# Kernel optimization log

Measured on AMD Instinct MI355X. Metric: run time of the kernel, lower is better.

## Reference

```python
import jax, jax.numpy as jnp
import numpy as np

HW = 128  # BEV heatmap size hardcoded in the module

def conv2d(x, w, b, pad):
    y = jax.lax.conv_general_dilated(x, w, (1, 1), [(pad, pad), (pad, pad)],
                                     dimension_numbers=('NCHW', 'OIHW', 'NCHW'))
    return y + b[None, :, None, None]

def setup_inputs() -> dict:
    key = jax.random.key(0)
    ks = jax.random.split(key, 8)
    B, C, N = 4, 64, 4096
    middle_feat_lidar = jax.random.normal(ks[0], (B, C, HW, HW), dtype=jnp.float32)
    voxels_feat_radar = jax.random.normal(ks[1], (N, C), dtype=jnp.float32)
    rcoors = jax.random.randint(ks[2], (N, 4), 0, HW, dtype=jnp.int64)
    rcoors = rcoors.at[:, 0].set(rcoors[:, 0] % B)  # batch index in [0, B)
    rcs = jax.random.uniform(ks[3], (N,), dtype=jnp.float32) * 6.0
    gamma = jnp.array(1.0, dtype=jnp.float32)  # self.rcs_gamma
    # rcs_att: Conv2d(2, C, 1); compress: Conv2d(2C, C, 3, pad=1)
    att_w = jax.random.normal(ks[4], (C, 2, 1, 1), dtype=jnp.float32) * 0.5
    att_b = jnp.zeros((C,), dtype=jnp.float32)
    comp_w = jax.random.normal(ks[5], (C, 2 * C, 3, 3), dtype=jnp.float32) * (1.0 / np.sqrt(2 * C * 9))
    comp_b = jnp.zeros((C,), dtype=jnp.float32)
    return {"middle_feat_lidar": middle_feat_lidar, "voxels_feat_radar": voxels_feat_radar,
            "rcoors": rcoors, "batch_size": B, "rcs": rcs, "gamma": gamma,
            "att_w": att_w, "att_b": att_b, "comp_w": comp_w, "comp_b": comp_b}

def _draw_maps(rcoors, rcs, gamma, batch_size):
    # Vectorized CenterPoint-style gaussian scatter-max over all N points.
    true_rcs = jax.nn.relu(rcs)                      # (N,)
    r = jnp.floor(gamma * true_rcs + 1.0)            # int() truncation; radius >= 1
    sigma = (2.0 * r + 1.0) / 6.0                    # sigma = diameter / 6
    b = rcoors[:, 0]
    y = rcoors[:, 2].astype(jnp.float32)
    x = rcoors[:, 3].astype(jnp.float32)
    grid = jnp.arange(HW, dtype=jnp.float32)
    dy = grid[None, :] - y[:, None]                  # (N, HW) rows
    dx = grid[None, :] - x[:, None]                  # (N, HW) cols
    g = jnp.exp(-(dy[:, :, None] ** 2 + dx[:, None, :] ** 2)
                / (2.0 * sigma[:, None, None] ** 2))  # (N, HW, HW)
    eps = jnp.finfo(jnp.float32).eps
    g = jnp.where(g < eps, 0.0, g)                   # gaussian_2d eps cutoff (max is 1 at center)
    # truncate gaussian to its (2r+1) box, as the slicing in draw_heatmap_gaussian does
    box = (jnp.abs(dy[:, :, None]) <= r[:, None, None]) & (jnp.abs(dx[:, None, :]) <= r[:, None, None])
    g = jnp.where(box, g, 0.0)
    heatmap = jnp.maximum(jax.ops.segment_max(g, b, num_segments=batch_size), 0.0)          # (B,HW,HW)
    heatmap_feat = jnp.maximum(
        jax.ops.segment_max(g * true_rcs[:, None, None], b, num_segments=batch_size), 0.0)  # (B,HW,HW)
    return heatmap, heatmap_feat

def reference(middle_feat_lidar, voxels_feat_radar, rcoors, batch_size, rcs,
              gamma, att_w, att_b, comp_w, comp_b):
    heatmap, heatmap_feat = _draw_maps(rcoors, rcs, gamma, batch_size)
    hm2 = jnp.stack([heatmap, heatmap_feat], axis=1)        # (B,2,HW,HW)
    rcs_features = conv2d(hm2, att_w, att_b, pad=0)          # 1x1 conv
    fused = jnp.concatenate([middle_feat_lidar, rcs_features], axis=1)
    return conv2d(fused, comp_w, comp_b, pad=1)              # 3x3 conv
```

## Files before the change

### kernel.cpp

```cpp
#include <hip/hip_runtime.h>
#include <math.h>

#define HW 128
#define CCH 64

typedef unsigned short u16;
typedef __attribute__((ext_vector_type(8))) short bf16x8;
typedef __attribute__((ext_vector_type(4))) float f32x4;

static __device__ __forceinline__ u16 f2bf(float x) {
    unsigned int u = __float_as_uint(x);
    unsigned int r = (u + 0x7FFFu + ((u >> 16) & 1u)) >> 16;
    return (u16)r;
}

__global__ void splat_kernel(const int* __restrict__ rcoors,
                             const float* __restrict__ rcs,
                             const float* __restrict__ gamma_p,
                             float* __restrict__ Hm, float* __restrict__ Fm,
                             int N, int B) {
    int n = blockIdx.x;
    if (n >= N) return;
    int b  = rcoors[n * 4 + 0];
    int yi = rcoors[n * 4 + 2];
    int xi = rcoors[n * 4 + 3];
    if ((unsigned)b >= (unsigned)B) return;
    float tr = fmaxf(rcs[n], 0.0f);
    float gamma = gamma_p[0];
    float r = floorf(gamma * tr + 1.0f);
    float sigma = (2.0f * r + 1.0f) * (1.0f / 6.0f);
    float inv2s2 = 1.0f / (2.0f * sigma * sigma);
    int R = (int)r;
    int W = 2 * R + 1;
    int tot = W * W;
    float y = (float)yi, x = (float)xi;
    for (int cell = threadIdx.x; cell < tot; cell += blockDim.x) {
        int cy = cell / W;
        int cx = cell - cy * W;
        int iy = yi - R + cy;
        int ix = xi - R + cx;
        if ((unsigned)iy >= HW || (unsigned)ix >= HW) continue;
        float dy = (float)iy - y, dx = (float)ix - x;
        float g = expf(-(dy * dy + dx * dx) * inv2s2);
        if (g < 1.1920929e-7f) continue;
        int idx = (b * HW + iy) * HW + ix;
        atomicMax((int*)&Hm[idx], __float_as_int(g));
        float gf = g * tr;
        if (gf > 0.0f) atomicMax((int*)&Fm[idx], __float_as_int(gf));
    }
}

__global__ void fold_kernel(const float* __restrict__ comp_w,
                            const float* __restrict__ att_w,
                            const float* __restrict__ att_b,
                            float* __restrict__ wH, float* __restrict__ wF,
                            float* __restrict__ wB) {
    int tid = blockIdx.x * blockDim.x + threadIdx.x;
    if (tid >= CCH * 9) return;
    int co = tid / 9, t = tid - co * 9;
    float sH = 0.f, sF = 0.f, sB = 0.f;
    for (int c2 = 0; c2 < CCH; ++c2) {
        float w = comp_w[((size_t)co * (2 * CCH) + (CCH + c2)) * 9 + t];
        sH += w * att_w[c2 * 2 + 0];
        sF += w * att_w[c2 * 2 + 1];
        sB += w * att_b[c2];
    }
    wH[tid] = sH; wF[tid] = sF; wB[tid] = sB;
}

__global__ void packw_kernel(const float* __restrict__ comp_w,
                             const float* __restrict__ wH,
                             const float* __restrict__ wF,
                             const float* __restrict__ wB,
                             u16* __restrict__ Wp) {
    int idx = blockIdx.x * 256 + threadIdx.x;
    if (idx >= 64 * 672) return;
    int co = idx / 672, k = idx - co * 672;
    int oct = k >> 3, j = k & 7;
    u16 v = 0;
    if (oct < 81) {
        int t = oct / 9, o = oct - t * 9;
        int ci = o * 8 + j;
        float w = 0.0f;
        if (ci < 64)       w = comp_w[((size_t)co * 128 + ci) * 9 + t];
        else if (ci == 64) w = wH[co * 9 + t];
        else if (ci == 65) w = wF[co * 9 + t];
        else if (ci == 66) w = wB[co * 9 + t];
        v = f2bf(w);
    }
    Wp[idx] = v;
}

__global__ void xpose_kernel(const float* __restrict__ middle,
                             u16* __restrict__ Xg) {
    int y = blockIdx.x, b = blockIdx.y;
    int tid = threadIdx.x;
    __shared__ u16 T[128 * 72];
    for (int it = 0; it < 32; ++it) {
        int idx = it * 256 + tid;
        int ci = idx >> 7, x = idx & 127;
        float v = middle[(((size_t)b * 64 + ci) * HW + y) * HW + x];
        T[x * 72 + ci] = f2bf(v);
    }
    __syncthreads();
    u16* dst = Xg + ((size_t)(b * HW + y) * HW) * 64;
    for (int it = 0; it < 8; ++it) {
        int idx = it * 256 + tid;
        int x = idx >> 4, c4 = idx & 15;
        uint2 v = *(const uint2*)(T + x * 72 + c4 * 4);
        *(uint2*)(dst + x * 64 + c4 * 4) = v;
    }
}

__global__ __launch_bounds__(256)
void conv_kernel(const u16* __restrict__ Xg,
                 const float* __restrict__ Hm, const float* __restrict__ Fm,
                 const u16* __restrict__ Wp, const float* __restrict__ comp_b,
                 float* __restrict__ out) {
    const int bx = blockIdx.x, by = blockIdx.y, b = blockIdx.z;
    const int tid = threadIdx.x;
    const int wave = tid >> 6, lane = tid & 63;
    const int col = lane & 15, quad = lane >> 4;
    const int i0 = by * 16 - 1, j0 = bx * 16 - 1;

    __shared__ u16 Xs[18 * 18 * 72];

    {
        const u16* XgB = Xg + (size_t)b * HW * HW * 64;
        const float* HmB = Hm + b * HW * HW;
        const float* FmB = Fm + b * HW * HW;
        for (int u = tid; u < 324 * 9; u += 256) {
            int site = u / 9, slot = u - site * 9;
            int rr = site / 18, cc = site - rr * 18;
            int gi = i0 + rr, gj = j0 + cc;
            bool in = ((unsigned)gi < HW) && ((unsigned)gj < HW);
            uint4 v = make_uint4(0u, 0u, 0u, 0u);
            if (slot < 8) {
                if (in) v = *(const uint4*)(XgB + ((gi * HW + gj) * 64 + slot * 8));
            } else {
                if (in) {
                    int p = gi * HW + gj;
                    u16 hb = f2bf(HmB[p]);
                    u16 fb = f2bf(FmB[p]);
                    v.x = (unsigned)hb | ((unsigned)fb << 16);
                    v.y = 0x3F80u;
                }
            }
            *(uint4*)(Xs + site * 72 + slot * 8) = v;
        }
    }
    __syncthreads();

    f32x4 acc[4][4];
#pragma unroll
    for (int m = 0; m < 4; ++m)
#pragma unroll
        for (int n = 0; n < 4; ++n) acc[m][n] = (f32x4){0.f, 0.f, 0.f, 0.f};

#pragma unroll
    for (int c = 0; c < 21; ++c) {
        bf16x8 af[4];
#pragma unroll
        for (int m = 0; m < 4; ++m)
            af[m] = *(const bf16x8*)(Wp + (m * 16 + col) * 672 + c * 32 + quad * 8);

        int oct = c * 4 + quad;
        if (oct > 80) oct = 80;
        int t  = oct / 9;
        int o  = oct - t * 9;
        int dy = t / 3, dx = t - dy * 3;
        int base = ((wave * 4 + dy) * 18 + (col + dx)) * 72 + o * 8;

        bf16x8 bfr[4];
#pragma unroll
        for (int n = 0; n < 4; ++n)
            bfr[n] = *(const bf16x8*)(Xs + base + n * (18 * 72));

#pragma unroll
        for (int m = 0; m < 4; ++m)
#pragma unroll
            for (int n = 0; n < 4; ++n)
                acc[m][n] = __builtin_amdgcn_mfma_f32_16x16x32_bf16(af[m], bfr[n], acc[m][n], 0, 0, 0);
    }

#pragma unroll
    for (int m = 0; m < 4; ++m) {
        int co0 = m * 16 + quad * 4;
#pragma unroll
        for (int n = 0; n < 4; ++n) {
            int i = by * 16 + wave * 4 + n;
            int j = bx * 16 + col;
            float* o0 = out + (((size_t)(b * 64 + co0) * HW + i) * HW + j);
#pragma unroll
            for (int r = 0; r < 4; ++r)
                o0[(size_t)r * HW * HW] = acc[m][n][r] + comp_b[co0 + r];
        }
    }
}

extern "C" void kernel_launch(void* const* d_in, const int* in_sizes, int n_in,
                              void* d_out, int out_size, void* d_ws, size_t ws_size,
                              hipStream_t stream) {
    const float* middle  = (const float*)d_in[0];
    const int*   rcoors  = (const int*)d_in[2];
    const float* rcs     = (const float*)d_in[4];
    const float* gamma   = (const float*)d_in[5];
    const float* att_w   = (const float*)d_in[6];
    const float* att_b   = (const float*)d_in[7];
    const float* comp_w  = (const float*)d_in[8];
    const float* comp_b  = (const float*)d_in[9];
    float* out = (float*)d_out;

    int B = in_sizes[0] / (CCH * HW * HW);
    int N = in_sizes[4];

    float* Hm = (float*)d_ws;
    float* Fm = Hm + (size_t)B * HW * HW;
    float* wH = Fm + (size_t)B * HW * HW;
    float* wF = wH + CCH * 9;
    float* wB = wF + CCH * 9;
    u16*   Wp = (u16*)(wB + CCH * 9);
    u16*   Xg = Wp + 64 * 672;

    hipMemsetAsync(Hm, 0, (size_t)2 * B * HW * HW * sizeof(float), stream);
    fold_kernel<<<dim3((CCH * 9 + 255) / 256), 256, 0, stream>>>(comp_w, att_w, att_b, wH, wF, wB);
    packw_kernel<<<dim3((64 * 672 + 255) / 256), 256, 0, stream>>>(comp_w, wH, wF, wB, Wp);
    splat_kernel<<<dim3(N), 64, 0, stream>>>(rcoors, rcs, gamma, Hm, Fm, N, B);
    xpose_kernel<<<dim3(HW, B), 256, 0, stream>>>(middle, Xg);
    conv_kernel<<<dim3(8, 8, B), 256, 0, stream>>>(Xg, Hm, Fm, Wp, comp_b, out);
}
```

Baseline: 120.9 us.

## Merge prep launches and double conv block threads to 512

Folds the memset, weight-fold and weight-pack steps into one prep kernel, and merges the transpose and gaussian splat into one heterogeneous work kernel. This cuts the launch count from six to three. The conv kernel now runs 8 waves per block, each computing 2 output rows instead of 4, which raises parallelism on the 256-block grid but halves per-wave reuse of the weight fragments. The splat blocks now have 256 threads instead of 64, so most lanes sit idle for small radii.

```diff
diff --git a/kernel.cpp b/kernel.cpp
--- a/kernel.cpp
+++ b/kernel.cpp
@@ -14,105 +14,99 @@
     return (u16)r;
 }
 
-__global__ void splat_kernel(const int* __restrict__ rcoors,
-                             const float* __restrict__ rcs,
-                             const float* __restrict__ gamma_p,
-                             float* __restrict__ Hm, float* __restrict__ Fm,
-                             int N, int B) {
-    int n = blockIdx.x;
-    if (n >= N) return;
-    int b  = rcoors[n * 4 + 0];
-    int yi = rcoors[n * 4 + 2];
-    int xi = rcoors[n * 4 + 3];
-    if ((unsigned)b >= (unsigned)B) return;
-    float tr = fmaxf(rcs[n], 0.0f);
-    float gamma = gamma_p[0];
-    float r = floorf(gamma * tr + 1.0f);
-    float sigma = (2.0f * r + 1.0f) * (1.0f / 6.0f);
-    float inv2s2 = 1.0f / (2.0f * sigma * sigma);
-    int R = (int)r;
-    int W = 2 * R + 1;
-    int tot = W * W;
-    float y = (float)yi, x = (float)xi;
-    for (int cell = threadIdx.x; cell < tot; cell += blockDim.x) {
-        int cy = cell / W;
-        int cx = cell - cy * W;
-        int iy = yi - R + cy;
-        int ix = xi - R + cx;
-        if ((unsigned)iy >= HW || (unsigned)ix >= HW) continue;
-        float dy = (float)iy - y, dx = (float)ix - x;
-        float g = expf(-(dy * dy + dx * dx) * inv2s2);
-        if (g < 1.1920929e-7f) continue;
-        int idx = (b * HW + iy) * HW + ix;
-        atomicMax((int*)&Hm[idx], __float_as_int(g));
-        float gf = g * tr;
-        if (gf > 0.0f) atomicMax((int*)&Fm[idx], __float_as_int(gf));
-    }
-}
-
-__global__ void fold_kernel(const float* __restrict__ comp_w,
+__global__ void prep_kernel(const float* __restrict__ comp_w,
                             const float* __restrict__ att_w,
                             const float* __restrict__ att_b,
-                            float* __restrict__ wH, float* __restrict__ wF,
-                            float* __restrict__ wB) {
-    int tid = blockIdx.x * blockDim.x + threadIdx.x;
-    if (tid >= CCH * 9) return;
-    int co = tid / 9, t = tid - co * 9;
-    float sH = 0.f, sF = 0.f, sB = 0.f;
-    for (int c2 = 0; c2 < CCH; ++c2) {
-        float w = comp_w[((size_t)co * (2 * CCH) + (CCH + c2)) * 9 + t];
-        sH += w * att_w[c2 * 2 + 0];
-        sF += w * att_w[c2 * 2 + 1];
-        sB += w * att_b[c2];
-    }
-    wH[tid] = sH; wF[tid] = sF; wB[tid] = sB;
-}
-
-__global__ void packw_kernel(const float* __restrict__ comp_w,
-                             const float* __restrict__ wH,
-                             const float* __restrict__ wF,
-                             const float* __restrict__ wB,
-                             u16* __restrict__ Wp) {
-    int idx = blockIdx.x * 256 + threadIdx.x;
-    if (idx >= 64 * 672) return;
-    int co = idx / 672, k = idx - co * 672;
-    int oct = k >> 3, j = k & 7;
-    u16 v = 0;
-    if (oct < 81) {
-        int t = oct / 9, o = oct - t * 9;
-        int ci = o * 8 + j;
-        float w = 0.0f;
-        if (ci < 64)       w = comp_w[((size_t)co * 128 + ci) * 9 + t];
-        else if (ci == 64) w = wH[co * 9 + t];
-        else if (ci == 65) w = wF[co * 9 + t];
-        else if (ci == 66) w = wB[co * 9 + t];
-        v = f2bf(w);
-    }
-    Wp[idx] = v;
-}
-
-__global__ void xpose_kernel(const float* __restrict__ middle,
-                             u16* __restrict__ Xg) {
-    int y = blockIdx.x, b = blockIdx.y;
-    int tid = threadIdx.x;
-    __shared__ u16 T[128 * 72];
-    for (int it = 0; it < 32; ++it) {
-        int idx = it * 256 + tid;
-        int ci = idx >> 7, x = idx & 127;
-        float v = middle[(((size_t)b * 64 + ci) * HW + y) * HW + x];
-        T[x * 72 + ci] = f2bf(v);
-    }
-    __syncthreads();
-    u16* dst = Xg + ((size_t)(b * HW + y) * HW) * 64;
-    for (int it = 0; it < 8; ++it) {
-        int idx = it * 256 + tid;
-        int x = idx >> 4, c4 = idx & 15;
-        uint2 v = *(const uint2*)(T + x * 72 + c4 * 4);
-        *(uint2*)(dst + x * 64 + c4 * 4) = v;
-    }
-}
-
-__global__ __launch_bounds__(256)
+                            float* __restrict__ Hm, u16* __restrict__ Wp,
+                            int ZB) {
+    int blk = blockIdx.x, tid = threadIdx.x;
+    if (blk < ZB) {
+        ((float4*)Hm)[blk * 256 + tid] = make_float4(0.f, 0.f, 0.f, 0.f);
+        return;
+    }
+    int pid = (blk - ZB) * 256 + tid;
+    for (int idx = pid; idx < 64 * 672; idx += 64 * 256) {
+        int co = idx / 672, k = idx - co * 672;
+        int oct = k >> 3, j = k & 7;
+        u16 v = 0;
+        if (oct < 81) {
+            int t = oct / 9, o = oct - t * 9;
+            int ci = o * 8 + j;
+            float w = 0.0f;
+            if (ci < 64) {
+                w = comp_w[((size_t)co * 128 + ci) * 9 + t];
+            } else if (ci < 67) {
+                float s = 0.f;
+                for (int c2 = 0; c2 < 64; ++c2) {
+                    float ww = comp_w[((size_t)co * 128 + 64 + c2) * 9 + t];
+                    float a = (ci == 64) ? att_w[c2 * 2 + 0]
+                            : (ci == 65) ? att_w[c2 * 2 + 1]
+                                         : att_b[c2];
+                    s = fmaf(ww, a, s);
+                }
+                w = s;
+            }
+            v = f2bf(w);
+        }
+        Wp[idx] = v;
+    }
+}
+
+__global__ void work_kernel(const float* __restrict__ middle,
+                            const int* __restrict__ rcoors,
+                            const float* __restrict__ rcs,
+                            const float* __restrict__ gamma_p,
+                            float* __restrict__ Hm, float* __restrict__ Fm,
+                            u16* __restrict__ Xg, int N, int B) {
+    int blk = blockIdx.x, tid = threadIdx.x;
+    int XB = B * HW;
+    if (blk < XB) {
+        int y = blk & (HW - 1), b = blk >> 7;
+        __shared__ u16 T[HW * 72];
+        for (int it = 0; it < 32; ++it) {
+            int idx = it * 256 + tid;
+            int ci = idx >> 7, x = idx & 127;
+            T[x * 72 + ci] = f2bf(middle[(((size_t)b * 64 + ci) * HW + y) * HW + x]);
+        }
+        __syncthreads();
+        u16* dst = Xg + (size_t)(b * HW + y) * HW * 64;
+        for (int it = 0; it < 8; ++it) {
+            int idx = it * 256 + tid;
+            int x = idx >> 4, c4 = idx & 15;
+            *(uint2*)(dst + x * 64 + c4 * 4) = *(const uint2*)(T + x * 72 + c4 * 4);
+        }
+    } else {
+        int n = blk - XB;
+        if (n >= N) return;
+        int b  = rcoors[n * 4 + 0];
+        int yi = rcoors[n * 4 + 2];
+        int xi = rcoors[n * 4 + 3];
+        if ((unsigned)b >= (unsigned)B) return;
+        float tr = fmaxf(rcs[n], 0.0f);
+        float r = floorf(gamma_p[0] * tr + 1.0f);
+        float sigma = (2.0f * r + 1.0f) * (1.0f / 6.0f);
+        float inv2s2 = 1.0f / (2.0f * sigma * sigma);
+        int R = (int)r;
+        int W = 2 * R + 1;
+        int tot = W * W;
+        for (int cell = tid; cell < tot; cell += 256) {
+            int cy = cell / W;
+            int cx = cell - cy * W;
+            int iy = yi - R + cy;
+            int ix = xi - R + cx;
+            if ((unsigned)iy >= HW || (unsigned)ix >= HW) continue;
+            float dy = (float)(iy - yi), dx = (float)(ix - xi);
+            float g = expf(-(dy * dy + dx * dx) * inv2s2);
+            if (g < 1.1920929e-7f) continue;
+            int idx = (b * HW + iy) * HW + ix;
+            atomicMax((int*)&Hm[idx], __float_as_int(g));
+            float gf = g * tr;
+            if (gf > 0.0f) atomicMax((int*)&Fm[idx], __float_as_int(gf));
+        }
+    }
+}
+
+__global__ __launch_bounds__(512)
 void conv_kernel(const u16* __restrict__ Xg,
                  const float* __restrict__ Hm, const float* __restrict__ Fm,
                  const u16* __restrict__ Wp, const float* __restrict__ comp_b,
@@ -129,7 +123,7 @@
         const u16* XgB = Xg + (size_t)b * HW * HW * 64;
         const float* HmB = Hm + b * HW * HW;
         const float* FmB = Fm + b * HW * HW;
-        for (int u = tid; u < 324 * 9; u += 256) {
+        for (int u = tid; u < 324 * 9; u += 512) {
             int site = u / 9, slot = u - site * 9;
             int rr = site / 18, cc = site - rr * 18;
             int gi = i0 + rr, gj = j0 + cc;
@@ -137,25 +131,21 @@
             uint4 v = make_uint4(0u, 0u, 0u, 0u);
             if (slot < 8) {
                 if (in) v = *(const uint4*)(XgB + ((gi * HW + gj) * 64 + slot * 8));
-            } else {
-                if (in) {
-                    int p = gi * HW + gj;
-                    u16 hb = f2bf(HmB[p]);
-                    u16 fb = f2bf(FmB[p]);
-                    v.x = (unsigned)hb | ((unsigned)fb << 16);
-                    v.y = 0x3F80u;
-                }
+            } else if (in) {
+                int p = gi * HW + gj;
+                v.x = (unsigned)f2bf(HmB[p]) | ((unsigned)f2bf(FmB[p]) << 16);
+                v.y = 0x3F80u;
             }
             *(uint4*)(Xs + site * 72 + slot * 8) = v;
         }
     }
     __syncthreads();
 
-    f32x4 acc[4][4];
+    f32x4 acc[4][2];
 #pragma unroll
     for (int m = 0; m < 4; ++m)
 #pragma unroll
-        for (int n = 0; n < 4; ++n) acc[m][n] = (f32x4){0.f, 0.f, 0.f, 0.f};
+        for (int n = 0; n < 2; ++n) acc[m][n] = (f32x4){0.f, 0.f, 0.f, 0.f};
 
 #pragma unroll
     for (int c = 0; c < 21; ++c) {
@@ -169,17 +159,17 @@
         int t  = oct / 9;
         int o  = oct - t * 9;
         int dy = t / 3, dx = t - dy * 3;
-        int base = ((wave * 4 + dy) * 18 + (col + dx)) * 72 + o * 8;
-
-        bf16x8 bfr[4];
-#pragma unroll
-        for (int n = 0; n < 4; ++n)
-            bfr[n] = *(const bf16x8*)(Xs + base + n * (18 * 72));
+        const u16* Bb = Xs + ((wave * 2 + dy) * 18 + (col + dx)) * 72 + o * 8;
+
+        bf16x8 bfr[2];
+#pragma unroll
+        for (int n = 0; n < 2; ++n)
+            bfr[n] = *(const bf16x8*)(Bb + n * (18 * 72));
 
 #pragma unroll
         for (int m = 0; m < 4; ++m)
 #pragma unroll
-            for (int n = 0; n < 4; ++n)
+            for (int n = 0; n < 2; ++n)
                 acc[m][n] = __builtin_amdgcn_mfma_f32_16x16x32_bf16(af[m], bfr[n], acc[m][n], 0, 0, 0);
     }
 
@@ -187,8 +177,8 @@
     for (int m = 0; m < 4; ++m) {
         int co0 = m * 16 + quad * 4;
 #pragma unroll
-        for (int n = 0; n < 4; ++n) {
-            int i = by * 16 + wave * 4 + n;
+        for (int n = 0; n < 2; ++n) {
+            int i = by * 16 + wave * 2 + n;
             int j = bx * 16 + col;
             float* o0 = out + (((size_t)(b * 64 + co0) * HW + i) * HW + j);
 #pragma unroll
@@ -216,16 +206,11 @@
 
     float* Hm = (float*)d_ws;
     float* Fm = Hm + (size_t)B * HW * HW;
-    float* wH = Fm + (size_t)B * HW * HW;
-    float* wF = wH + CCH * 9;
-    float* wB = wF + CCH * 9;
-    u16*   Wp = (u16*)(wB + CCH * 9);
+    u16*   Wp = (u16*)(Fm + (size_t)B * HW * HW);
     u16*   Xg = Wp + 64 * 672;
 
-    hipMemsetAsync(Hm, 0, (size_t)2 * B * HW * HW * sizeof(float), stream);
-    fold_kernel<<<dim3((CCH * 9 + 255) / 256), 256, 0, stream>>>(comp_w, att_w, att_b, wH, wF, wB);
-    packw_kernel<<<dim3((64 * 672 + 255) / 256), 256, 0, stream>>>(comp_w, wH, wF, wB, Wp);
-    splat_kernel<<<dim3(N), 64, 0, stream>>>(rcoors, rcs, gamma, Hm, Fm, N, B);
-    xpose_kernel<<<dim3(HW, B), 256, 0, stream>>>(middle, Xg);
-    conv_kernel<<<dim3(8, 8, B), 256, 0, stream>>>(Xg, Hm, Fm, Wp, comp_b, out);
-}
+    int ZB = (2 * B * HW * HW) / 1024;
+    prep_kernel<<<dim3(ZB + 64), 256, 0, stream>>>(comp_w, att_w, att_b, Hm, Wp, ZB);
+    work_kernel<<<dim3(B * HW + N), 256, 0, stream>>>(middle, rcoors, rcs, gamma, Hm, Fm, Xg, N, B);
+    conv_kernel<<<dim3(8, 8, B), 512, 0, stream>>>(Xg, Hm, Fm, Wp, comp_b, out);
+}
```

Measured after the change: 138.8 us. 1.15x slower.
